# Kernel tuning notes

Measured on AMD Instinct MI355X. Metric: run time of the kernel, lower is better.

## Reference

```python
import jax, jax.numpy as jnp
import numpy as np

B, N, DIM, HEADS, DEPTH, MLP = 4, 1024, 256, 4, 4, 1024
DH = DIM // HEADS
EPS = 1e-5


def _ln(x, g, b):
    mu = jnp.mean(x, axis=-1, keepdims=True)
    var = jnp.mean((x - mu) ** 2, axis=-1, keepdims=True)
    return (x - mu) / jnp.sqrt(var + EPS) * g + b


def setup_inputs() -> dict:
    key = jax.random.key(0)
    ks = jax.random.split(key, 10)
    s = 0.02
    p = {}
    p["x"] = jax.random.normal(ks[0], (B, N, DIM), jnp.float32)
    p["attn_bias"] = jax.random.normal(ks[1], (2, B, HEADS, N, N), jnp.float32)
    p["ln1_g"] = jnp.ones((DEPTH, DIM), jnp.float32)
    p["ln1_b"] = jnp.zeros((DEPTH, DIM), jnp.float32)
    p["Wkv"] = jax.random.normal(ks[2], (DEPTH, DIM, 2 * DIM), jnp.float32) * s
    p["Wq"] = jax.random.normal(ks[3], (DEPTH, DIM, DIM), jnp.float32) * s
    p["Wo"] = jax.random.normal(ks[4], (DEPTH, DIM, DIM), jnp.float32) * s
    p["bo"] = jnp.zeros((DEPTH, DIM), jnp.float32)
    p["ln2_g"] = jnp.ones((DEPTH, DIM), jnp.float32)
    p["ln2_b"] = jnp.zeros((DEPTH, DIM), jnp.float32)
    p["W1"] = jax.random.normal(ks[5], (DEPTH, DIM, MLP), jnp.float32) * s
    p["b1"] = jnp.zeros((DEPTH, MLP), jnp.float32)
    p["W2"] = jax.random.normal(ks[6], (DEPTH, MLP, DIM), jnp.float32) * s
    p["b2"] = jnp.zeros((DEPTH, DIM), jnp.float32)
    p["Wg"] = jax.random.normal(ks[7], (DIM, DIM), jnp.float32) * s
    p["lng_g"] = jnp.ones((DIM,), jnp.float32)
    p["lng_b"] = jnp.zeros((DIM,), jnp.float32)
    return p


def reference(x, attn_bias, ln1_g, ln1_b, Wkv, Wq, Wo, bo, ln2_g, ln2_b, W1, b1, W2, b2, Wg, lng_g, lng_b):
    scale = DIM ** -0.5
    add_attn = attn_bias[0] + attn_bias[1]            # [B,H,N,N]
    # aggregation bias matrices are layer-invariant (recomputed identically each layer in torch)
    A = jnp.mean(attn_bias[0], axis=1)                # [B,N,N]
    S = jnp.mean(attn_bias[1], axis=1)
    G = jax.nn.softmax(A * S, axis=2)                 # [B,N,N]

    def split_heads(t):  # [B,N,DIM] -> [B,H,N,DH]
        return t.reshape(B, N, HEADS, DH).transpose(0, 2, 1, 3)

    for l in range(DEPTH):
        # softmax-GCN aggregation
        x_ma = jax.nn.relu(_ln(jnp.matmul(G, x) @ Wg, lng_g, lng_b))
        # attention (PreNorm on x only; q comes from un-normed x_ma)
        xn = _ln(x, ln1_g[l], ln1_b[l])
        kv = xn @ Wkv[l]
        k, v = jnp.split(kv, 2, axis=-1)
        q = x_ma @ Wq[l]
        qh, kh, vh = split_heads(q), split_heads(k), split_heads(v)
        dots = jnp.einsum('bhid,bhjd->bhij', qh, kh) * scale + add_attn
        attn = jax.nn.softmax(dots, axis=-1)
        out = jnp.einsum('bhij,bhjd->bhid', attn, vh)
        out = out.transpose(0, 2, 1, 3).reshape(B, N, DIM)
        x = x + out @ Wo[l] + bo[l]
        # feed-forward (exact GELU, matching torch nn.GELU default)
        xn2 = _ln(x, ln2_g[l], ln2_b[l])
        x = x + jax.nn.gelu(xn2 @ W1[l] + b1[l], approximate=False) @ W2[l] + b2[l]
    return x
```

## Files before the change

### kernel.cpp

```cpp
#include <hip/hip_runtime.h>
#include <hip/hip_bf16.h>
#include <math.h>

typedef unsigned short u16;
typedef __bf16 bf16x8 __attribute__((ext_vector_type(8)));
typedef float f32x4 __attribute__((ext_vector_type(4)));

#define B_ 4
#define N_ 1024
#define DIM_ 256
#define HEADS_ 4
#define DH_ 64
#define MLP_ 1024
#define DEPTH_ 4

__device__ __forceinline__ float r2f(u16 r){ return __uint_as_float(((unsigned)r)<<16); }
__device__ __forceinline__ u16 f2r(float f){ __hip_bfloat16 h = __float2bfloat16(f); return *(u16*)&h; }

__device__ __forceinline__ float gelu_exact(float v){
  return 0.5f*v*(1.0f + erff(v*0.70710678118654752440f));
}

#define MFMA16(a,b,c) __builtin_amdgcn_mfma_f32_16x16x32_bf16(a,b,c,0,0,0)

__global__ void prep_bias(const float* __restrict__ bias, u16* __restrict__ G, u16* __restrict__ bsum){
  int blk = blockIdx.x;
  int i = blk & (N_-1);
  int b = blk >> 10;
  int t = threadIdx.x;
  __shared__ float red[256];
  long long base0 = ((long long)(b*HEADS_)*N_ + i)*(long long)N_;
  const long long hs = (long long)N_*N_;
  const long long cs = (long long)B_*HEADS_*N_*N_;
  int j0 = t*4;
  f32x4 a = {0.f,0.f,0.f,0.f}, s = {0.f,0.f,0.f,0.f};
  #pragma unroll
  for (int h=0;h<HEADS_;h++){
    f32x4 x0 = *(const f32x4*)(bias + base0 + h*hs + j0);
    f32x4 x1 = *(const f32x4*)(bias + cs + base0 + h*hs + j0);
    a += x0; s += x1;
    union { ushort4 u; u16 e[4]; } pk;
    #pragma unroll
    for (int k=0;k<4;k++) pk.e[k] = f2r(x0[k]+x1[k]);
    *(ushort4*)(bsum + base0 + h*hs + j0) = pk.u;
  }
  float v[4]; float lmax = -3e38f;
  #pragma unroll
  for (int k=0;k<4;k++){ v[k] = (a[k]*0.25f)*(s[k]*0.25f); lmax = fmaxf(lmax, v[k]); }
  red[t]=lmax; __syncthreads();
  for (int st=128;st>0;st>>=1){ if(t<st) red[t]=fmaxf(red[t],red[t+st]); __syncthreads(); }
  float m = red[0]; __syncthreads();
  float e[4]; float lsum = 0.f;
  #pragma unroll
  for (int k=0;k<4;k++){ e[k] = __expf(v[k]-m); lsum += e[k]; }
  red[t]=lsum; __syncthreads();
  for (int st=128;st>0;st>>=1){ if(t<st) red[t]+=red[t+st]; __syncthreads(); }
  float inv = 1.0f/red[0];
  u16* Grow = G + ((long long)b*N_ + i)*(long long)N_;
  union { ushort4 u; u16 e[4]; } pg;
  #pragma unroll
  for (int k=0;k<4;k++) pg.e[k] = f2r(e[k]*inv);
  *(ushort4*)(Grow + j0) = pg.u;
}

__global__ void ln_kernel(const float* __restrict__ X, u16* __restrict__ Y,
                          const float* __restrict__ g, const float* __restrict__ bvec){
  int row = blockIdx.x*8 + (threadIdx.x>>5);
  int cg = threadIdx.x&31;
  const float* xp = X + (long long)row*DIM_ + cg*8;
  f32x4 v0 = *(const f32x4*)xp;
  f32x4 v1 = *(const f32x4*)(xp+4);
  float s = v0[0]+v0[1]+v0[2]+v0[3]+v1[0]+v1[1]+v1[2]+v1[3];
  s += __shfl_xor(s,1); s += __shfl_xor(s,2); s += __shfl_xor(s,4); s += __shfl_xor(s,8); s += __shfl_xor(s,16);
  float mu = s*(1.0f/256.0f);
  float s2 = 0.f;
  #pragma unroll
  for (int k=0;k<4;k++){ float d=v0[k]-mu; s2 += d*d; }
  #pragma unroll
  for (int k=0;k<4;k++){ float d=v1[k]-mu; s2 += d*d; }
  s2 += __shfl_xor(s2,1); s2 += __shfl_xor(s2,2); s2 += __shfl_xor(s2,4); s2 += __shfl_xor(s2,8); s2 += __shfl_xor(s2,16);
  float rstd = rsqrtf(s2*(1.0f/256.0f)+1e-5f);
  f32x4 g0 = *(const f32x4*)(g + cg*8);
  f32x4 g1 = *(const f32x4*)(g + cg*8 + 4);
  f32x4 b0 = *(const f32x4*)(bvec + cg*8);
  f32x4 b1 = *(const f32x4*)(bvec + cg*8 + 4);
  union { ushort4 u[2]; u16 e[8]; } pk;
  #pragma unroll
  for (int k=0;k<4;k++) pk.e[k]   = f2r((v0[k]-mu)*rstd*g0[k] + b0[k]);
  #pragma unroll
  for (int k=0;k<4;k++) pk.e[4+k] = f2r((v1[k]-mu)*rstd*g1[k] + b1[k]);
  u16* yp = Y + (long long)row*DIM_ + cg*8;
  *(ushort4*)yp = pk.u[0];
  *(ushort4*)(yp+4) = pk.u[1];
}

__global__ void tcast_all(const float* __restrict__ Wkv, const float* __restrict__ Wq,
                          const float* __restrict__ Wo, const float* __restrict__ W1,
                          const float* __restrict__ W2, const float* __restrict__ Wg,
                          const float* __restrict__ xin,
                          u16* WkvT, u16* WqT, u16* WoT, u16* W1T, u16* W2T, u16* WgT, u16* xT){
  int z = blockIdx.z;
  const float* I; u16* O; int ldin, R, C;
  if (z < 4)       { I = Wkv + z*131072;      O = WkvT + z*131072;      ldin=512;  R=256;  C=512;  }
  else if (z < 8)  { I = Wq  + (z-4)*65536;   O = WqT  + (z-4)*65536;   ldin=256;  R=256;  C=256;  }
  else if (z < 12) { I = Wo  + (z-8)*65536;   O = WoT  + (z-8)*65536;   ldin=256;  R=256;  C=256;  }
  else if (z < 16) { I = W1  + (z-12)*262144; O = W1T  + (z-12)*262144; ldin=1024; R=256;  C=1024; }
  else if (z < 20) { I = W2  + (z-16)*262144; O = W2T  + (z-16)*262144; ldin=256;  R=1024; C=256;  }
  else if (z == 20){ I = Wg;                  O = WgT;                  ldin=256;  R=256;  C=256;  }
  else             { I = xin + (z-21)*262144; O = xT   + (z-21)*262144; ldin=256;  R=1024; C=256;  }
  int c0 = blockIdx.x*32, r0 = blockIdx.y*32;
  if (c0 >= C || r0 >= R) return;
  __shared__ float tile[32][33];
  int tx = threadIdx.x, ty = threadIdx.y;
  #pragma unroll
  for (int i=0;i<4;i++)
    tile[ty*4+i][tx] = I[(long long)(r0+ty*4+i)*ldin + c0+tx];
  __syncthreads();
  #pragma unroll
  for (int i=0;i<4;i++)
    O[(long long)(c0+ty*4+i)*R + r0+tx] = f2r(tile[tx][ty*4+i]);
}

__global__ __launch_bounds__(512) void layer_pre(
    const u16* __restrict__ Gb, const u16* __restrict__ xT, const u16* __restrict__ xnb,
    const u16* __restrict__ WgT, const u16* __restrict__ WqT, const u16* __restrict__ WkvT,
    const float* __restrict__ lng, const float* __restrict__ lnb,
    u16* __restrict__ qb, u16* __restrict__ kvb, u16* __restrict__ vt)
{
  __shared__ float Gx_s[16][264];
  __shared__ float t2_s[16][264];
  __shared__ u16  xma_s[16][264];
  int tid = threadIdx.x;
  int w = tid>>6, lane = tid&63, lr = lane&15, qd = lane>>4;
  int row0 = blockIdx.x*16;
  int batch = row0>>10, brow0 = row0&1023;

  {
    int kw = w>>2, cw = w&3;
    const u16* Ap = Gb + (long long)batch*1048576 + (long long)(brow0+lr)*1024 + kw*512;
    const u16* Bp = xT + (long long)batch*262144 + (long long)kw*512;
    f32x4 acc[4] = {};
    for (int k0=0;k0<512;k0+=32){
      bf16x8 af = *(const bf16x8*)(Ap + k0 + qd*8);
      #pragma unroll
      for (int nt=0;nt<4;nt++){
        bf16x8 bf = *(const bf16x8*)(Bp + (long long)(cw*64+nt*16+lr)*1024 + k0 + qd*8);
        acc[nt] = MFMA16(af,bf,acc[nt]);
      }
    }
    if (kw==0){
      #pragma unroll
      for (int nt=0;nt<4;nt++)
        #pragma unroll
        for (int r=0;r<4;r++) Gx_s[qd*4+r][cw*64+nt*16+lr] = acc[nt][r];
    }
    __syncthreads();
    if (kw==1){
      #pragma unroll
      for (int nt=0;nt<4;nt++)
        #pragma unroll
        for (int r=0;r<4;r++) Gx_s[qd*4+r][cw*64+nt*16+lr] += acc[nt][r];
    }
    __syncthreads();
  }
  {
    int r = tid>>5, cg = tid&31;
    #pragma unroll
    for (int i=0;i<8;i++) xma_s[r][cg*8+i] = f2r(Gx_s[r][cg*8+i]);
  }
  __syncthreads();
  {
    f32x4 acc[2] = {};
    for (int k0=0;k0<256;k0+=32){
      bf16x8 af = *(const bf16x8*)&xma_s[lr][k0+qd*8];
      #pragma unroll
      for (int i=0;i<2;i++){
        bf16x8 bf = *(const bf16x8*)(WgT + (long long)((w*2+i)*16+lr)*256 + k0 + qd*8);
        acc[i] = MFMA16(af,bf,acc[i]);
      }
    }
    #pragma unroll
    for (int i=0;i<2;i++)
      #pragma unroll
      for (int r=0;r<4;r++) t2_s[qd*4+r][(w*2+i)*16+lr] = acc[i][r];
  }
  __syncthreads();
  {
    int r = tid>>5, cg = tid&31;
    float v[8]; float s=0.f;
    #pragma unroll
    for (int i=0;i<8;i++){ v[i] = t2_s[r][cg*8+i]; s += v[i]; }
    s += __shfl_xor(s,1); s += __shfl_xor(s,2); s += __shfl_xor(s,4); s += __shfl_xor(s,8); s += __shfl_xor(s,16);
    float mu = s*(1.0f/256.0f);
    float s2=0.f;
    #pragma unroll
    for (int i=0;i<8;i++){ float d=v[i]-mu; s2 += d*d; }
    s2 += __shfl_xor(s2,1); s2 += __shfl_xor(s2,2); s2 += __shfl_xor(s2,4); s2 += __shfl_xor(s2,8); s2 += __shfl_xor(s2,16);
    float rstd = rsqrtf(s2*(1.0f/256.0f)+1e-5f);
    #pragma unroll
    for (int i=0;i<8;i++){
      int c = cg*8+i;
      float y = (v[i]-mu)*rstd*lng[c] + lnb[c];
      xma_s[r][c] = f2r(fmaxf(y,0.f));
    }
  }
  __syncthreads();
  {
    f32x4 acc[2] = {};
    for (int k0=0;k0<256;k0+=32){
      bf16x8 af = *(const bf16x8*)&xma_s[lr][k0+qd*8];
      #pragma unroll
      for (int i=0;i<2;i++){
        bf16x8 bf = *(const bf16x8*)(WqT + (long long)((w*2+i)*16+lr)*256 + k0 + qd*8);
        acc[i] = MFMA16(af,bf,acc[i]);
      }
    }
    #pragma unroll
    for (int i=0;i<2;i++)
      #pragma unroll
      for (int r=0;r<4;r++)
        qb[(long long)(row0+qd*4+r)*DIM_ + (w*2+i)*16+lr] = f2r(acc[i][r]);
  }
  {
    const u16* Ap = xnb + (long long)(row0+lr)*DIM_;
    f32x4 acc[4] = {};
    for (int k0=0;k0<256;k0+=32){
      bf16x8 af = *(const bf16x8*)(Ap + k0 + qd*8);
      #pragma unroll
      for (int i=0;i<4;i++){
        bf16x8 bf = *(const bf16x8*)(WkvT + (long long)((w*4+i)*16+lr)*256 + k0 + qd*8);
        acc[i] = MFMA16(af,bf,acc[i]);
      }
    }
    #pragma unroll
    for (int i=0;i<4;i++){
      int col = (w*4+i)*16+lr;
      #pragma unroll
      for (int r=0;r<4;r++){
        int row = row0+qd*4+r;
        float v = acc[i][r];
        kvb[(long long)row*512 + col] = f2r(v);
        if (col >= 256)
          vt[(long long)batch*262144 + (long long)(col-256)*1024 + (row&1023)] = f2r(v);
      }
    }
  }
}

__global__ __launch_bounds__(512) void flash_attn(
    const u16* __restrict__ qb, const u16* __restrict__ kvb,
    const u16* __restrict__ vt, const u16* __restrict__ bsum,
    u16* __restrict__ out)
{
  int z = blockIdx.z;
  int b = z>>2, h = z&3;
  int qt = blockIdx.x;
  int tid = threadIdx.x;
  int w = tid>>6, lane = tid&63;
  int g = w>>2, tw = w&3;
  int lr = lane&15, qd = lane>>4;
  __shared__ u16 Pl[8][16][72];
  __shared__ u16 sb[8][16][72];
  __shared__ float Ol[8][16][68];
  __shared__ float Ml[8][16];
  __shared__ float Ll[8][16];

  int qrow0 = qt*64 + tw*16;
  const u16* qp = qb + ((long long)(b*N_) + qrow0 + lr)*DIM_ + h*DH_;
  bf16x8 aq0 = *(const bf16x8*)(qp + qd*8);
  bf16x8 aq1 = *(const bf16x8*)(qp + 32 + qd*8);

  f32x4 oacc[4] = {};
  float m_r[4] = {-3e38f,-3e38f,-3e38f,-3e38f};
  float l_r[4] = {0.f,0.f,0.f,0.f};

  const u16* kbase = kvb + ((long long)(b*N_))*512 + h*DH_;
  const u16* vbase = vt + (long long)b*(DIM_*N_) + (long long)(h*DH_)*N_;
  const u16* bias_base = bsum + ((long long)z*N_ + qrow0)*(long long)N_;
  int srr = lane>>2, scc = (lane&3)*16;

  for (int jtl=0; jtl<8; jtl++){
    int j0 = (g*8 + jtl)*64;
    {
      const u16* gs = bias_base + (long long)srr*N_ + j0 + scc;
      uint4 t0 = *(const uint4*)gs;
      uint4 t1 = *(const uint4*)(gs+8);
      *(uint4*)&sb[w][srr][scc]   = t0;
      *(uint4*)&sb[w][srr][scc+8] = t1;
    }
    f32x4 sacc[4] = {};
    #pragma unroll
    for (int nt=0; nt<4; nt++){
      const u16* kp = kbase + (long long)(j0 + nt*16 + lr)*512;
      bf16x8 bk0 = *(const bf16x8*)(kp + qd*8);
      bf16x8 bk1 = *(const bf16x8*)(kp + 32 + qd*8);
      sacc[nt] = MFMA16(aq0, bk0, sacc[nt]);
      sacc[nt] = MFMA16(aq1, bk1, sacc[nt]);
    }
    #pragma unroll
    for (int r=0;r<4;r++){
      float pv[4];
      float vmax = -3e38f;
      #pragma unroll
      for (int nt=0;nt<4;nt++){
        float v = sacc[nt][r]*0.0625f + r2f(sb[w][qd*4+r][nt*16+lr]);
        pv[nt] = v;
        vmax = fmaxf(vmax, v);
      }
      vmax = fmaxf(vmax, __shfl_xor(vmax,1));
      vmax = fmaxf(vmax, __shfl_xor(vmax,2));
      vmax = fmaxf(vmax, __shfl_xor(vmax,4));
      vmax = fmaxf(vmax, __shfl_xor(vmax,8));
      float newm = fmaxf(m_r[r], vmax);
      float alpha = __expf(m_r[r]-newm);
      m_r[r] = newm;
      float psum = 0.f;
      #pragma unroll
      for (int nt=0;nt<4;nt++){
        float p = __expf(pv[nt]-newm);
        psum += p;
        Pl[w][qd*4+r][nt*16+lr] = f2r(p);
      }
      psum += __shfl_xor(psum,1);
      psum += __shfl_xor(psum,2);
      psum += __shfl_xor(psum,4);
      psum += __shfl_xor(psum,8);
      l_r[r] = l_r[r]*alpha + psum;
      #pragma unroll
      for (int ot=0;ot<4;ot++) oacc[ot][r] *= alpha;
    }
    #pragma unroll
    for (int ks=0;ks<2;ks++){
      bf16x8 ap = *(const bf16x8*)&Pl[w][lr][ks*32 + qd*8];
      #pragma unroll
      for (int ot=0;ot<4;ot++){
        const u16* vp = vbase + (long long)(ot*16+lr)*N_ + j0 + ks*32 + qd*8;
        bf16x8 bv = *(const bf16x8*)vp;
        oacc[ot] = MFMA16(ap, bv, oacc[ot]);
      }
    }
  }
  #pragma unroll
  for (int r=0;r<4;r++){
    int row = qd*4+r;
    #pragma unroll
    for (int ot=0;ot<4;ot++) Ol[w][row][ot*16+lr] = oacc[ot][r];
    if (lr==0){ Ml[w][row] = m_r[r]; Ll[w][row] = l_r[r]; }
  }
  __syncthreads();
  if (w < 4){
    #pragma unroll
    for (int r=0;r<4;r++){
      int row = qd*4+r;
      float m0 = Ml[w][row], m1 = Ml[w+4][row];
      float mm = fmaxf(m0,m1);
      float e0 = __expf(m0-mm), e1 = __expf(m1-mm);
      float inv = 1.0f/(Ll[w][row]*e0 + Ll[w+4][row]*e1);
      #pragma unroll
      for (int ot=0;ot<4;ot++){
        float o = Ol[w][row][ot*16+lr]*e0 + Ol[w+4][row][ot*16+lr]*e1;
        out[((long long)(b*N_) + qrow0 + row)*DIM_ + h*DH_ + ot*16 + lr] = f2r(o*inv);
      }
    }
  }
}

__global__ __launch_bounds__(512) void layer_post(
    const u16* __restrict__ aob, const float* __restrict__ resx,
    const u16* __restrict__ WoT, const float* __restrict__ bo,
    const float* __restrict__ ln2g, const float* __restrict__ ln2b,
    const u16* __restrict__ W1T, const float* __restrict__ b1,
    const u16* __restrict__ W2T, const float* __restrict__ b2,
    float* __restrict__ xf_out,
    const float* __restrict__ ln1g_next, const float* __restrict__ ln1b_next,
    u16* __restrict__ xn_out, u16* __restrict__ xT_out)
{
  __shared__ float v_s[16][264];
  __shared__ u16  xn2_s[16][264];
  __shared__ u16  h1_s[16][1048];
  __shared__ float xnew_s[16][264];
  int tid = threadIdx.x;
  int w = tid>>6, lane = tid&63, lr = lane&15, qd = lane>>4;
  int row0 = blockIdx.x*16;
  int batch = row0>>10;

  {
    const u16* Ap = aob + (long long)(row0+lr)*DIM_;
    f32x4 acc[2] = {};
    for (int k0=0;k0<256;k0+=32){
      bf16x8 af = *(const bf16x8*)(Ap + k0 + qd*8);
      #pragma unroll
      for (int i=0;i<2;i++){
        bf16x8 bf = *(const bf16x8*)(WoT + (long long)((w*2+i)*16+lr)*256 + k0 + qd*8);
        acc[i] = MFMA16(af,bf,acc[i]);
      }
    }
    #pragma unroll
    for (int i=0;i<2;i++){
      int col = (w*2+i)*16+lr;
      #pragma unroll
      for (int r=0;r<4;r++)
        v_s[qd*4+r][col] = acc[i][r] + bo[col] + resx[(long long)(row0+qd*4+r)*DIM_ + col];
    }
  }
  __syncthreads();
  {
    int r = tid>>5, cg = tid&31;
    float v[8]; float s=0.f;
    #pragma unroll
    for (int i=0;i<8;i++){ v[i] = v_s[r][cg*8+i]; s += v[i]; }
    s += __shfl_xor(s,1); s += __shfl_xor(s,2); s += __shfl_xor(s,4); s += __shfl_xor(s,8); s += __shfl_xor(s,16);
    float mu = s*(1.0f/256.0f);
    float s2=0.f;
    #pragma unroll
    for (int i=0;i<8;i++){ float d=v[i]-mu; s2 += d*d; }
    s2 += __shfl_xor(s2,1); s2 += __shfl_xor(s2,2); s2 += __shfl_xor(s2,4); s2 += __shfl_xor(s2,8); s2 += __shfl_xor(s2,16);
    float rstd = rsqrtf(s2*(1.0f/256.0f)+1e-5f);
    #pragma unroll
    for (int i=0;i<8;i++){
      int c = cg*8+i;
      xn2_s[r][c] = f2r((v[i]-mu)*rstd*ln2g[c] + ln2b[c]);
    }
  }
  __syncthreads();
  {
    f32x4 acc[8] = {};
    for (int k0=0;k0<256;k0+=32){
      bf16x8 af = *(const bf16x8*)&xn2_s[lr][k0+qd*8];
      #pragma unroll
      for (int i=0;i<8;i++){
        bf16x8 bf = *(const bf16x8*)(W1T + (long long)((w*8+i)*16+lr)*256 + k0 + qd*8);
        acc[i] = MFMA16(af,bf,acc[i]);
      }
    }
    #pragma unroll
    for (int i=0;i<8;i++){
      int col = (w*8+i)*16+lr;
      #pragma unroll
      for (int r=0;r<4;r++)
        h1_s[qd*4+r][col] = f2r(gelu_exact(acc[i][r] + b1[col]));
    }
  }
  __syncthreads();
  {
    f32x4 acc[2] = {};
    for (int k0=0;k0<1024;k0+=32){
      bf16x8 af = *(const bf16x8*)&h1_s[lr][k0+qd*8];
      #pragma unroll
      for (int i=0;i<2;i++){
        bf16x8 bf = *(const bf16x8*)(W2T + (long long)((w*2+i)*16+lr)*1024 + k0 + qd*8);
        acc[i] = MFMA16(af,bf,acc[i]);
      }
    }
    #pragma unroll
    for (int i=0;i<2;i++){
      int col = (w*2+i)*16+lr;
      #pragma unroll
      for (int r=0;r<4;r++){
        float v = acc[i][r] + b2[col] + v_s[qd*4+r][col];
        xf_out[(long long)(row0+qd*4+r)*DIM_ + col] = v;
        xnew_s[qd*4+r][col] = v;
      }
    }
  }
  if (ln1g_next){
    __syncthreads();
    int r = tid>>5, cg = tid&31;
    float v[8]; float s=0.f;
    #pragma unroll
    for (int i=0;i<8;i++){ v[i] = xnew_s[r][cg*8+i]; s += v[i]; }
    s += __shfl_xor(s,1); s += __shfl_xor(s,2); s += __shfl_xor(s,4); s += __shfl_xor(s,8); s += __shfl_xor(s,16);
    float mu = s*(1.0f/256.0f);
    float s2=0.f;
    #pragma unroll
    for (int i=0;i<8;i++){ float d=v[i]-mu; s2 += d*d; }
    s2 += __shfl_xor(s2,1); s2 += __shfl_xor(s2,2); s2 += __shfl_xor(s2,4); s2 += __shfl_xor(s2,8); s2 += __shfl_xor(s2,16);
    float rstd = rsqrtf(s2*(1.0f/256.0f)+1e-5f);
    int grow = row0 + r;
    #pragma unroll
    for (int i=0;i<8;i++){
      int c = cg*8+i;
      xn_out[(long long)grow*DIM_ + c] = f2r((v[i]-mu)*rstd*ln1g_next[c] + ln1b_next[c]);
      xT_out[(long long)batch*262144 + (long long)c*1024 + (grow&1023)] = f2r(v[i]);
    }
  }
}

extern "C" void kernel_launch(void* const* d_in, const int* in_sizes, int n_in,
                              void* d_out, int out_size, void* d_ws, size_t ws_size,
                              hipStream_t stream){
  const float* x_in   = (const float*)d_in[0];
  const float* abias  = (const float*)d_in[1];
  const float* ln1_g  = (const float*)d_in[2];
  const float* ln1_b  = (const float*)d_in[3];
  const float* Wkv    = (const float*)d_in[4];
  const float* Wq     = (const float*)d_in[5];
  const float* Wo     = (const float*)d_in[6];
  const float* bo     = (const float*)d_in[7];
  const float* ln2_g  = (const float*)d_in[8];
  const float* ln2_b  = (const float*)d_in[9];
  const float* W1     = (const float*)d_in[10];
  const float* b1     = (const float*)d_in[11];
  const float* W2     = (const float*)d_in[12];
  const float* b2     = (const float*)d_in[13];
  const float* Wg     = (const float*)d_in[14];
  const float* lng_g  = (const float*)d_in[15];
  const float* lng_b  = (const float*)d_in[16];

  char* ws = (char*)d_ws;
  float* xf   = (float*)(ws);
  u16*  Gb    = (u16*)(ws + (4ll<<20));
  u16*  bsum  = (u16*)(ws + (12ll<<20));
  u16*  kvb   = (u16*)(ws + (44ll<<20));
  u16*  vt    = (u16*)(ws + (48ll<<20));
  u16*  xT    = (u16*)(ws + (50ll<<20));
  u16*  xnb   = (u16*)(ws + (52ll<<20));
  u16*  qb    = (u16*)(ws + (54ll<<20));
  u16*  aob   = (u16*)(ws + (56ll<<20));
  u16*  WkvT  = (u16*)(ws + (58ll<<20));
  u16*  WqT   = (u16*)(ws + (59ll<<20));
  u16*  WoT   = (u16*)(ws + (59ll<<20) + (512ll<<10));
  u16*  W1T   = (u16*)(ws + (60ll<<20));
  u16*  W2T   = (u16*)(ws + (62ll<<20));
  u16*  WgT   = (u16*)(ws + (64ll<<20));

  dim3 b256(256), b512(512);

  prep_bias<<<dim3(B_*N_), b256, 0, stream>>>(abias, Gb, bsum);
  tcast_all<<<dim3(32,32,25), dim3(32,8), 0, stream>>>(Wkv,Wq,Wo,W1,W2,Wg,x_in,
                                                       WkvT,WqT,WoT,W1T,W2T,WgT,xT);
  ln_kernel<<<dim3(512), b256, 0, stream>>>(x_in, xnb, ln1_g, ln1_b);

  for (int l=0; l<DEPTH_; l++){
    const float* resx = (l==0) ? x_in : xf;
    layer_pre<<<dim3(256), b512, 0, stream>>>(Gb, xT, xnb,
        WgT, WqT + (long long)l*65536, WkvT + (long long)l*131072,
        lng_g, lng_b, qb, kvb, vt);
    flash_attn<<<dim3(16,1,B_*HEADS_), b512, 0, stream>>>(qb, kvb, vt, bsum, aob);
    if (l < DEPTH_-1){
      layer_post<<<dim3(256), b512, 0, stream>>>(aob, resx,
          WoT + (long long)l*65536, bo + l*DIM_, ln2_g + l*DIM_, ln2_b + l*DIM_,
          W1T + (long long)l*262144, b1 + l*MLP_, W2T + (long long)l*262144, b2 + l*DIM_,
          xf, ln1_g + (l+1)*DIM_, ln1_b + (l+1)*DIM_, xnb, xT);
    } else {
      layer_post<<<dim3(256), b512, 0, stream>>>(aob, resx,
          WoT + (long long)l*65536, bo + l*DIM_, ln2_g + l*DIM_, ln2_b + l*DIM_,
          W1T + (long long)l*262144, b1 + l*MLP_, W2T + (long long)l*262144, b2 + l*DIM_,
          (float*)d_out, nullptr, nullptr, nullptr, nullptr);
    }
  }
}
```

Measured before the change: 760.9 us.

## Fuse flash attention into post-layer kernel and split KV projection into separate blocks

The flash-attention kernel is merged into the post-attention kernel. Each 16-row block computes attention for all four heads (two waves per head, each taking half the keys), combines the partial softmax results in shared memory, and feeds the output straight into the Wo/FFN path, so the global aob round-trip and one launch per layer go away. The KV projection moves out of layer_pre into extra blocks (grid doubled to 512) that run alongside the GCN/Q blocks. A shared-memory union is added with a new barrier to guard the aliased buffers. Attention parallelism drops from 256 blocks of 64 query rows to 256 blocks of 16 rows that each cover all heads, which changes load balance and makes every block walk the full key range for every head.

```diff
diff --git a/kernel.cpp b/kernel.cpp
--- a/kernel.cpp
+++ b/kernel.cpp
@@ -121,7 +121,7 @@
     O[(long long)(c0+ty*4+i)*R + r0+tx] = f2r(tile[tx][ty*4+i]);
 }
 
-__global__ __launch_bounds__(512) void layer_pre(
+__global__ __launch_bounds__(512, 4) void layer_pre(
     const u16* __restrict__ Gb, const u16* __restrict__ xT, const u16* __restrict__ xnb,
     const u16* __restrict__ WgT, const u16* __restrict__ WqT, const u16* __restrict__ WkvT,
     const float* __restrict__ lng, const float* __restrict__ lnb,
@@ -132,7 +132,37 @@
   __shared__ u16  xma_s[16][264];
   int tid = threadIdx.x;
   int w = tid>>6, lane = tid&63, lr = lane&15, qd = lane>>4;
-  int row0 = blockIdx.x*16;
+  int bid = blockIdx.x;
+
+  if (bid >= 256){
+    int row0 = (bid-256)*16;
+    int batch = row0>>10;
+    const u16* Ap = xnb + (long long)(row0+lr)*DIM_;
+    f32x4 acc[4] = {};
+    for (int k0=0;k0<256;k0+=32){
+      bf16x8 af = *(const bf16x8*)(Ap + k0 + qd*8);
+      #pragma unroll
+      for (int i=0;i<4;i++){
+        bf16x8 bf = *(const bf16x8*)(WkvT + (long long)((w*4+i)*16+lr)*256 + k0 + qd*8);
+        acc[i] = MFMA16(af,bf,acc[i]);
+      }
+    }
+    #pragma unroll
+    for (int i=0;i<4;i++){
+      int col = (w*4+i)*16+lr;
+      #pragma unroll
+      for (int r=0;r<4;r++){
+        int row = row0+qd*4+r;
+        float v = acc[i][r];
+        kvb[(long long)row*512 + col] = f2r(v);
+        if (col >= 256)
+          vt[(long long)batch*262144 + (long long)(col-256)*1024 + (row&1023)] = f2r(v);
+      }
+    }
+    return;
+  }
+
+  int row0 = bid*16;
   int batch = row0>>10, brow0 = row0&1023;
 
   {
@@ -164,9 +194,9 @@
     __syncthreads();
   }
   {
-    int r = tid>>5, cg = tid&31;
-    #pragma unroll
-    for (int i=0;i<8;i++) xma_s[r][cg*8+i] = f2r(Gx_s[r][cg*8+i]);
+    int r = tid>>5, cg2 = tid&31;
+    #pragma unroll
+    for (int i=0;i<8;i++) xma_s[r][cg2*8+i] = f2r(Gx_s[r][cg2*8+i]);
   }
   __syncthreads();
   {
@@ -186,10 +216,10 @@
   }
   __syncthreads();
   {
-    int r = tid>>5, cg = tid&31;
+    int r = tid>>5, cg2 = tid&31;
     float v[8]; float s=0.f;
     #pragma unroll
-    for (int i=0;i<8;i++){ v[i] = t2_s[r][cg*8+i]; s += v[i]; }
+    for (int i=0;i<8;i++){ v[i] = t2_s[r][cg2*8+i]; s += v[i]; }
     s += __shfl_xor(s,1); s += __shfl_xor(s,2); s += __shfl_xor(s,4); s += __shfl_xor(s,8); s += __shfl_xor(s,16);
     float mu = s*(1.0f/256.0f);
     float s2=0.f;
@@ -199,7 +229,7 @@
     float rstd = rsqrtf(s2*(1.0f/256.0f)+1e-5f);
     #pragma unroll
     for (int i=0;i<8;i++){
-      int c = cg*8+i;
+      int c = cg2*8+i;
       float y = (v[i]-mu)*rstd*lng[c] + lnb[c];
       xma_s[r][c] = f2r(fmaxf(y,0.f));
     }
@@ -221,152 +251,13 @@
       for (int r=0;r<4;r++)
         qb[(long long)(row0+qd*4+r)*DIM_ + (w*2+i)*16+lr] = f2r(acc[i][r]);
   }
-  {
-    const u16* Ap = xnb + (long long)(row0+lr)*DIM_;
-    f32x4 acc[4] = {};
-    for (int k0=0;k0<256;k0+=32){
-      bf16x8 af = *(const bf16x8*)(Ap + k0 + qd*8);
-      #pragma unroll
-      for (int i=0;i<4;i++){
-        bf16x8 bf = *(const bf16x8*)(WkvT + (long long)((w*4+i)*16+lr)*256 + k0 + qd*8);
-        acc[i] = MFMA16(af,bf,acc[i]);
-      }
-    }
-    #pragma unroll
-    for (int i=0;i<4;i++){
-      int col = (w*4+i)*16+lr;
-      #pragma unroll
-      for (int r=0;r<4;r++){
-        int row = row0+qd*4+r;
-        float v = acc[i][r];
-        kvb[(long long)row*512 + col] = f2r(v);
-        if (col >= 256)
-          vt[(long long)batch*262144 + (long long)(col-256)*1024 + (row&1023)] = f2r(v);
-      }
-    }
-  }
-}
-
-__global__ __launch_bounds__(512) void flash_attn(
+}
+
+#define APSMEM 72704
+__global__ __launch_bounds__(512, 2) void attn_post(
     const u16* __restrict__ qb, const u16* __restrict__ kvb,
     const u16* __restrict__ vt, const u16* __restrict__ bsum,
-    u16* __restrict__ out)
-{
-  int z = blockIdx.z;
-  int b = z>>2, h = z&3;
-  int qt = blockIdx.x;
-  int tid = threadIdx.x;
-  int w = tid>>6, lane = tid&63;
-  int g = w>>2, tw = w&3;
-  int lr = lane&15, qd = lane>>4;
-  __shared__ u16 Pl[8][16][72];
-  __shared__ u16 sb[8][16][72];
-  __shared__ float Ol[8][16][68];
-  __shared__ float Ml[8][16];
-  __shared__ float Ll[8][16];
-
-  int qrow0 = qt*64 + tw*16;
-  const u16* qp = qb + ((long long)(b*N_) + qrow0 + lr)*DIM_ + h*DH_;
-  bf16x8 aq0 = *(const bf16x8*)(qp + qd*8);
-  bf16x8 aq1 = *(const bf16x8*)(qp + 32 + qd*8);
-
-  f32x4 oacc[4] = {};
-  float m_r[4] = {-3e38f,-3e38f,-3e38f,-3e38f};
-  float l_r[4] = {0.f,0.f,0.f,0.f};
-
-  const u16* kbase = kvb + ((long long)(b*N_))*512 + h*DH_;
-  const u16* vbase = vt + (long long)b*(DIM_*N_) + (long long)(h*DH_)*N_;
-  const u16* bias_base = bsum + ((long long)z*N_ + qrow0)*(long long)N_;
-  int srr = lane>>2, scc = (lane&3)*16;
-
-  for (int jtl=0; jtl<8; jtl++){
-    int j0 = (g*8 + jtl)*64;
-    {
-      const u16* gs = bias_base + (long long)srr*N_ + j0 + scc;
-      uint4 t0 = *(const uint4*)gs;
-      uint4 t1 = *(const uint4*)(gs+8);
-      *(uint4*)&sb[w][srr][scc]   = t0;
-      *(uint4*)&sb[w][srr][scc+8] = t1;
-    }
-    f32x4 sacc[4] = {};
-    #pragma unroll
-    for (int nt=0; nt<4; nt++){
-      const u16* kp = kbase + (long long)(j0 + nt*16 + lr)*512;
-      bf16x8 bk0 = *(const bf16x8*)(kp + qd*8);
-      bf16x8 bk1 = *(const bf16x8*)(kp + 32 + qd*8);
-      sacc[nt] = MFMA16(aq0, bk0, sacc[nt]);
-      sacc[nt] = MFMA16(aq1, bk1, sacc[nt]);
-    }
-    #pragma unroll
-    for (int r=0;r<4;r++){
-      float pv[4];
-      float vmax = -3e38f;
-      #pragma unroll
-      for (int nt=0;nt<4;nt++){
-        float v = sacc[nt][r]*0.0625f + r2f(sb[w][qd*4+r][nt*16+lr]);
-        pv[nt] = v;
-        vmax = fmaxf(vmax, v);
-      }
-      vmax = fmaxf(vmax, __shfl_xor(vmax,1));
-      vmax = fmaxf(vmax, __shfl_xor(vmax,2));
-      vmax = fmaxf(vmax, __shfl_xor(vmax,4));
-      vmax = fmaxf(vmax, __shfl_xor(vmax,8));
-      float newm = fmaxf(m_r[r], vmax);
-      float alpha = __expf(m_r[r]-newm);
-      m_r[r] = newm;
-      float psum = 0.f;
-      #pragma unroll
-      for (int nt=0;nt<4;nt++){
-        float p = __expf(pv[nt]-newm);
-        psum += p;
-        Pl[w][qd*4+r][nt*16+lr] = f2r(p);
-      }
-      psum += __shfl_xor(psum,1);
-      psum += __shfl_xor(psum,2);
-      psum += __shfl_xor(psum,4);
-      psum += __shfl_xor(psum,8);
-      l_r[r] = l_r[r]*alpha + psum;
-      #pragma unroll
-      for (int ot=0;ot<4;ot++) oacc[ot][r] *= alpha;
-    }
-    #pragma unroll
-    for (int ks=0;ks<2;ks++){
-      bf16x8 ap = *(const bf16x8*)&Pl[w][lr][ks*32 + qd*8];
-      #pragma unroll
-      for (int ot=0;ot<4;ot++){
-        const u16* vp = vbase + (long long)(ot*16+lr)*N_ + j0 + ks*32 + qd*8;
-        bf16x8 bv = *(const bf16x8*)vp;
-        oacc[ot] = MFMA16(ap, bv, oacc[ot]);
-      }
-    }
-  }
-  #pragma unroll
-  for (int r=0;r<4;r++){
-    int row = qd*4+r;
-    #pragma unroll
-    for (int ot=0;ot<4;ot++) Ol[w][row][ot*16+lr] = oacc[ot][r];
-    if (lr==0){ Ml[w][row] = m_r[r]; Ll[w][row] = l_r[r]; }
-  }
-  __syncthreads();
-  if (w < 4){
-    #pragma unroll
-    for (int r=0;r<4;r++){
-      int row = qd*4+r;
-      float m0 = Ml[w][row], m1 = Ml[w+4][row];
-      float mm = fmaxf(m0,m1);
-      float e0 = __expf(m0-mm), e1 = __expf(m1-mm);
-      float inv = 1.0f/(Ll[w][row]*e0 + Ll[w+4][row]*e1);
-      #pragma unroll
-      for (int ot=0;ot<4;ot++){
-        float o = Ol[w][row][ot*16+lr]*e0 + Ol[w+4][row][ot*16+lr]*e1;
-        out[((long long)(b*N_) + qrow0 + row)*DIM_ + h*DH_ + ot*16 + lr] = f2r(o*inv);
-      }
-    }
-  }
-}
-
-__global__ __launch_bounds__(512) void layer_post(
-    const u16* __restrict__ aob, const float* __restrict__ resx,
+    const float* __restrict__ resx,
     const u16* __restrict__ WoT, const float* __restrict__ bo,
     const float* __restrict__ ln2g, const float* __restrict__ ln2b,
     const u16* __restrict__ W1T, const float* __restrict__ b1,
@@ -375,20 +266,131 @@
     const float* __restrict__ ln1g_next, const float* __restrict__ ln1b_next,
     u16* __restrict__ xn_out, u16* __restrict__ xT_out)
 {
-  __shared__ float v_s[16][264];
-  __shared__ u16  xn2_s[16][264];
-  __shared__ u16  h1_s[16][1048];
-  __shared__ float xnew_s[16][264];
+  __shared__ __align__(16) char smem[APSMEM];
+  u16 (*sb)[16][72]   = (u16 (*)[16][72])smem;
+  u16 (*Pl)[16][72]   = (u16 (*)[16][72])(smem+18432);
+  float (*Ol)[16][68] = (float(*)[16][68])(smem+36864);
+  float (*Ml)[16]     = (float(*)[16])(smem+71680);
+  float (*Ll)[16]     = (float(*)[16])(smem+72192);
+  u16  (*ao_s)[264]   = (u16 (*)[264])smem;
+  float (*v_s)[264]   = (float(*)[264])(smem+8448);
+  u16  (*xn2_s)[264]  = (u16 (*)[264])(smem+25344);
+  u16  (*h1_s)[1048]  = (u16 (*)[1048])(smem+33792);
+  float (*xnew_s)[264]= (float(*)[264])(smem+33792);
+
   int tid = threadIdx.x;
   int w = tid>>6, lane = tid&63, lr = lane&15, qd = lane>>4;
   int row0 = blockIdx.x*16;
-  int batch = row0>>10;
-
-  {
-    const u16* Ap = aob + (long long)(row0+lr)*DIM_;
+  int batch = row0>>10, brow0 = row0&1023;
+
+  {
+    int h = w>>1, g = w&1;
+    int z = batch*HEADS_ + h;
+    const u16* qp = qb + ((long long)row0 + lr)*DIM_ + h*DH_;
+    bf16x8 aq0 = *(const bf16x8*)(qp + qd*8);
+    bf16x8 aq1 = *(const bf16x8*)(qp + 32 + qd*8);
+
+    f32x4 oacc[4] = {};
+    float m_r[4] = {-3e38f,-3e38f,-3e38f,-3e38f};
+    float l_r[4] = {0.f,0.f,0.f,0.f};
+
+    const u16* kbase = kvb + ((long long)(batch*N_))*512 + h*DH_;
+    const u16* vbase = vt + (long long)batch*(DIM_*N_) + (long long)(h*DH_)*N_;
+    const u16* bias_base = bsum + ((long long)z*N_ + brow0)*(long long)N_;
+    int srr = lane>>2, scc = (lane&3)*16;
+
+    for (int jtl=0; jtl<8; jtl++){
+      int j0 = (g*8 + jtl)*64;
+      {
+        const u16* gs = bias_base + (long long)srr*N_ + j0 + scc;
+        uint4 t0 = *(const uint4*)gs;
+        uint4 t1 = *(const uint4*)(gs+8);
+        *(uint4*)&sb[w][srr][scc]   = t0;
+        *(uint4*)&sb[w][srr][scc+8] = t1;
+      }
+      f32x4 sacc[4] = {};
+      #pragma unroll
+      for (int nt=0; nt<4; nt++){
+        const u16* kp = kbase + (long long)(j0 + nt*16 + lr)*512;
+        bf16x8 bk0 = *(const bf16x8*)(kp + qd*8);
+        bf16x8 bk1 = *(const bf16x8*)(kp + 32 + qd*8);
+        sacc[nt] = MFMA16(aq0, bk0, sacc[nt]);
+        sacc[nt] = MFMA16(aq1, bk1, sacc[nt]);
+      }
+      #pragma unroll
+      for (int r=0;r<4;r++){
+        float pv[4];
+        float vmax = -3e38f;
+        #pragma unroll
+        for (int nt=0;nt<4;nt++){
+          float v = sacc[nt][r]*0.0625f + r2f(sb[w][qd*4+r][nt*16+lr]);
+          pv[nt] = v;
+          vmax = fmaxf(vmax, v);
+        }
+        vmax = fmaxf(vmax, __shfl_xor(vmax,1));
+        vmax = fmaxf(vmax, __shfl_xor(vmax,2));
+        vmax = fmaxf(vmax, __shfl_xor(vmax,4));
+        vmax = fmaxf(vmax, __shfl_xor(vmax,8));
+        float newm = fmaxf(m_r[r], vmax);
+        float alpha = __expf(m_r[r]-newm);
+        m_r[r] = newm;
+        float psum = 0.f;
+        #pragma unroll
+        for (int nt=0;nt<4;nt++){
+          float p = __expf(pv[nt]-newm);
+          psum += p;
+          Pl[w][qd*4+r][nt*16+lr] = f2r(p);
+        }
+        psum += __shfl_xor(psum,1);
+        psum += __shfl_xor(psum,2);
+        psum += __shfl_xor(psum,4);
+        psum += __shfl_xor(psum,8);
+        l_r[r] = l_r[r]*alpha + psum;
+        #pragma unroll
+        for (int ot=0;ot<4;ot++) oacc[ot][r] *= alpha;
+      }
+      #pragma unroll
+      for (int ks=0;ks<2;ks++){
+        bf16x8 ap = *(const bf16x8*)&Pl[w][lr][ks*32 + qd*8];
+        #pragma unroll
+        for (int ot=0;ot<4;ot++){
+          const u16* vp = vbase + (long long)(ot*16+lr)*N_ + j0 + ks*32 + qd*8;
+          bf16x8 bv = *(const bf16x8*)vp;
+          oacc[ot] = MFMA16(ap, bv, oacc[ot]);
+        }
+      }
+    }
+    #pragma unroll
+    for (int r=0;r<4;r++){
+      int row = qd*4+r;
+      #pragma unroll
+      for (int ot=0;ot<4;ot++) Ol[w][row][ot*16+lr] = oacc[ot][r];
+      if (lr==0){ Ml[w][row] = m_r[r]; Ll[w][row] = l_r[r]; }
+    }
+  }
+  __syncthreads();
+  if (!(w&1)){
+    int h = w>>1;
+    #pragma unroll
+    for (int r=0;r<4;r++){
+      int row = qd*4+r;
+      float m0 = Ml[w][row], m1 = Ml[w+1][row];
+      float mm = fmaxf(m0,m1);
+      float e0 = __expf(m0-mm), e1 = __expf(m1-mm);
+      float inv = 1.0f/(Ll[w][row]*e0 + Ll[w+1][row]*e1);
+      #pragma unroll
+      for (int ot=0;ot<4;ot++){
+        float o = Ol[w][row][ot*16+lr]*e0 + Ol[w+1][row][ot*16+lr]*e1;
+        ao_s[row][h*DH_ + ot*16+lr] = f2r(o*inv);
+      }
+    }
+  }
+  __syncthreads();
+
+  {
     f32x4 acc[2] = {};
     for (int k0=0;k0<256;k0+=32){
-      bf16x8 af = *(const bf16x8*)(Ap + k0 + qd*8);
+      bf16x8 af = *(const bf16x8*)&ao_s[lr][k0+qd*8];
       #pragma unroll
       for (int i=0;i<2;i++){
         bf16x8 bf = *(const bf16x8*)(WoT + (long long)((w*2+i)*16+lr)*256 + k0 + qd*8);
@@ -405,10 +407,10 @@
   }
   __syncthreads();
   {
-    int r = tid>>5, cg = tid&31;
+    int r = tid>>5, cg2 = tid&31;
     float v[8]; float s=0.f;
     #pragma unroll
-    for (int i=0;i<8;i++){ v[i] = v_s[r][cg*8+i]; s += v[i]; }
+    for (int i=0;i<8;i++){ v[i] = v_s[r][cg2*8+i]; s += v[i]; }
     s += __shfl_xor(s,1); s += __shfl_xor(s,2); s += __shfl_xor(s,4); s += __shfl_xor(s,8); s += __shfl_xor(s,16);
     float mu = s*(1.0f/256.0f);
     float s2=0.f;
@@ -418,7 +420,7 @@
     float rstd = rsqrtf(s2*(1.0f/256.0f)+1e-5f);
     #pragma unroll
     for (int i=0;i<8;i++){
-      int c = cg*8+i;
+      int c = cg2*8+i;
       xn2_s[r][c] = f2r((v[i]-mu)*rstd*ln2g[c] + ln2b[c]);
     }
   }
@@ -452,6 +454,7 @@
         acc[i] = MFMA16(af,bf,acc[i]);
       }
     }
+    __syncthreads();
     #pragma unroll
     for (int i=0;i<2;i++){
       int col = (w*2+i)*16+lr;
@@ -465,10 +468,10 @@
   }
   if (ln1g_next){
     __syncthreads();
-    int r = tid>>5, cg = tid&31;
+    int r = tid>>5, cg2 = tid&31;
     float v[8]; float s=0.f;
     #pragma unroll
-    for (int i=0;i<8;i++){ v[i] = xnew_s[r][cg*8+i]; s += v[i]; }
+    for (int i=0;i<8;i++){ v[i] = xnew_s[r][cg2*8+i]; s += v[i]; }
     s += __shfl_xor(s,1); s += __shfl_xor(s,2); s += __shfl_xor(s,4); s += __shfl_xor(s,8); s += __shfl_xor(s,16);
     float mu = s*(1.0f/256.0f);
     float s2=0.f;
@@ -479,9 +482,9 @@
     int grow = row0 + r;
     #pragma unroll
     for (int i=0;i<8;i++){
-      int c = cg*8+i;
+      int c = cg2*8+i;
       xn_out[(long long)grow*DIM_ + c] = f2r((v[i]-mu)*rstd*ln1g_next[c] + ln1b_next[c]);
-      xT_out[(long long)batch*262144 + (long long)c*1024 + (grow&1023)] = f2r(v[i]);
+      xT_out[(long long)batch*262144 + (long long)c*1024 + ((grow)&1023)] = f2r(v[i]);
     }
   }
 }
@@ -516,7 +519,6 @@
   u16*  xT    = (u16*)(ws + (50ll<<20));
   u16*  xnb   = (u16*)(ws + (52ll<<20));
   u16*  qb    = (u16*)(ws + (54ll<<20));
-  u16*  aob   = (u16*)(ws + (56ll<<20));
   u16*  WkvT  = (u16*)(ws + (58ll<<20));
   u16*  WqT   = (u16*)(ws + (59ll<<20));
   u16*  WoT   = (u16*)(ws + (59ll<<20) + (512ll<<10));
@@ -524,26 +526,23 @@
   u16*  W2T   = (u16*)(ws + (62ll<<20));
   u16*  WgT   = (u16*)(ws + (64ll<<20));
 
-  dim3 b256(256), b512(512);
-
-  prep_bias<<<dim3(B_*N_), b256, 0, stream>>>(abias, Gb, bsum);
+  prep_bias<<<dim3(B_*N_), dim3(256), 0, stream>>>(abias, Gb, bsum);
   tcast_all<<<dim3(32,32,25), dim3(32,8), 0, stream>>>(Wkv,Wq,Wo,W1,W2,Wg,x_in,
                                                        WkvT,WqT,WoT,W1T,W2T,WgT,xT);
-  ln_kernel<<<dim3(512), b256, 0, stream>>>(x_in, xnb, ln1_g, ln1_b);
+  ln_kernel<<<dim3(512), dim3(256), 0, stream>>>(x_in, xnb, ln1_g, ln1_b);
 
   for (int l=0; l<DEPTH_; l++){
     const float* resx = (l==0) ? x_in : xf;
-    layer_pre<<<dim3(256), b512, 0, stream>>>(Gb, xT, xnb,
+    layer_pre<<<dim3(512), dim3(512), 0, stream>>>(Gb, xT, xnb,
         WgT, WqT + (long long)l*65536, WkvT + (long long)l*131072,
         lng_g, lng_b, qb, kvb, vt);
-    flash_attn<<<dim3(16,1,B_*HEADS_), b512, 0, stream>>>(qb, kvb, vt, bsum, aob);
     if (l < DEPTH_-1){
-      layer_post<<<dim3(256), b512, 0, stream>>>(aob, resx,
+      attn_post<<<dim3(256), dim3(512), 0, stream>>>(qb, kvb, vt, bsum, resx,
           WoT + (long long)l*65536, bo + l*DIM_, ln2_g + l*DIM_, ln2_b + l*DIM_,
           W1T + (long long)l*262144, b1 + l*MLP_, W2T + (long long)l*262144, b2 + l*DIM_,
           xf, ln1_g + (l+1)*DIM_, ln1_b + (l+1)*DIM_, xnb, xT);
     } else {
-      layer_post<<<dim3(256), b512, 0, stream>>>(aob, resx,
+      attn_post<<<dim3(256), dim3(512), 0, stream>>>(qb, kvb, vt, bsum, resx,
           WoT + (long long)l*65536, bo + l*DIM_, ln2_g + l*DIM_, ln2_b + l*DIM_,
           W1T + (long long)l*262144, b1 + l*MLP_, W2T + (long long)l*262144, b2 + l*DIM_,
           (float*)d_out, nullptr, nullptr, nullptr, nullptr);
```

Result: faster. 737.1 us (-3.1%).
